# Kernel tuning notes

Measured on AMD Instinct MI355X. Metric: run time of the kernel, lower is better.

## Reference

```python
import jax, jax.numpy as jnp
import numpy as np

BIT, RW, CW, YR, ID, ZC = 4, 8, 8, 512, 64, 512


def setup_inputs() -> dict:
    key = jax.random.key(0)
    ks = jax.random.split(key, 8)
    return {
        "X": jax.random.normal(ks[0], (4096, CW * ZC), dtype=jnp.float32),
        "Y": jax.random.uniform(ks[1], (BIT, RW, CW, YR, ID), dtype=jnp.float32),
        "Z": jax.random.uniform(ks[2], (BIT, RW, CW, ID, ZC), dtype=jnp.float32),
        "a": jax.random.normal(ks[3], (BIT, RW, CW, 1, 1), dtype=jnp.float32),
        "b": jax.random.normal(ks[4], (BIT, RW, CW, 1, 1), dtype=jnp.float32),
        "c": jax.random.normal(ks[5], (BIT, RW, CW, 1, 1), dtype=jnp.float32),
        "d": jax.random.normal(ks[6], (RW, CW, 1, 1), dtype=jnp.float32),
        "bias": jax.random.normal(ks[7], (RW * YR,), dtype=jnp.float32),
    }


def reference(X, Y, Z, a, b, c, d, bias):
    dtype = X.dtype
    # binary codebook buffers (registered as bool in torch): threshold at 0.5
    Yb = (Y > 0.5).astype(dtype)  # [bit, rw, cw, y_row, inter]
    Zb = (Z > 0.5).astype(dtype)  # [bit, rw, cw, inter, z_col]
    # batched binary matmul: [bit, rw, cw, y_row, z_col]
    W_core = jnp.einsum('brcyi,brciz->brcyz', Yb, Zb)
    Y_sum = jnp.sum(Yb, axis=-1, keepdims=True)  # [bit, rw, cw, y_row, 1]
    Z_sum = jnp.sum(Zb, axis=-2, keepdims=True)  # [bit, rw, cw, 1, z_col]
    W = a * W_core + b * Y_sum + c * Z_sum       # [bit, rw, cw, y_row, z_col]
    W = jnp.sum(W, axis=0) + d                   # [rw, cw, y_row, z_col]
    # permute(0,2,1,3) -> [rw, y_row, cw, z_col] -> [rw*y_row, cw*z_col]
    W = jnp.transpose(W, (0, 2, 1, 3)).reshape(RW * YR, CW * ZC)
    return X @ W.T + bias
```

## Files before the change

kernel.cpp:

```cpp
#include <hip/hip_runtime.h>

#define KDIM 4096
#define MDIM 4096
#define GAS __attribute__((address_space(1)))
#define LAS __attribute__((address_space(3)))

typedef __attribute__((ext_vector_type(8))) _Float16 f16x8;
typedef __attribute__((ext_vector_type(4))) float f32x4;

__device__ __forceinline__ unsigned short f2h(float v) {
    return __builtin_bit_cast(unsigned short, (_Float16)v);
}

__global__ __launch_bounds__(256) void pack_y_kernel(
    const float* __restrict__ Y, unsigned long long* __restrict__ Ym) {
    const int g = blockIdx.x * 4 + (threadIdx.x >> 6);
    const int lane = threadIdx.x & 63;
    float v = Y[(size_t)g * 64 + lane];
    unsigned long long m = __ballot(v > 0.5f);
    if (lane == 0) Ym[g] = m;
}

__global__ __launch_bounds__(512) void pack_z_kernel(
    const float* __restrict__ Z, unsigned long long* __restrict__ Zm) {
    const int s = blockIdx.x;
    const int z = threadIdx.x;
    const size_t base = (size_t)s * 64 * 512;
    unsigned long long m = 0;
#pragma unroll
    for (int i = 0; i < 64; ++i) {
        float v = Z[base + (size_t)i * 512 + z];
        m |= (unsigned long long)(v > 0.5f) << i;
    }
    Zm[(size_t)s * 512 + z] = m;
}

__global__ __launch_bounds__(512) void build_w_kernel(
    const unsigned long long* __restrict__ Ym, const unsigned long long* __restrict__ Zm,
    const float* __restrict__ Ac, const float* __restrict__ Bc,
    const float* __restrict__ Cc, const float* __restrict__ Dc,
    unsigned short* __restrict__ Wh) {
    const int rc = blockIdx.x;
    const int rw = rc >> 3, cw = rc & 7;
    const int yc = blockIdx.y;
    const int tid = threadIdx.x;
    const int zq = tid & 127;
    const int ys = tid >> 7;

    __shared__ unsigned long long sYm[4][16];

    float Ar[4], Br[4];
    float dval = Dc[rc];
    float czd4[4] = {dval, dval, dval, dval};
    unsigned long long zm[4][4];
#pragma unroll
    for (int b = 0; b < 4; ++b) {
        Ar[b] = Ac[b * 64 + rc];
        Br[b] = Bc[b * 64 + rc];
        float cb = Cc[b * 64 + rc];
        const unsigned long long* zp = Zm + (size_t)(b * 64 + rc) * 512 + zq * 4;
#pragma unroll
        for (int j = 0; j < 4; ++j) {
            zm[b][j] = zp[j];
            czd4[j] += cb * (float)__popcll(zm[b][j]);
        }
    }
    if (tid < 64)
        sYm[tid >> 4][tid & 15] = Ym[(size_t)((tid >> 4) * 64 + rc) * 512 + yc * 16 + (tid & 15)];
    __syncthreads();

#pragma unroll
    for (int yy = 0; yy < 4; ++yy) {
        const int yl = ys * 4 + yy;
        unsigned long long ym[4];
        float bt = 0.f;
#pragma unroll
        for (int b = 0; b < 4; ++b) {
            ym[b] = sYm[b][yl];
            bt += Br[b] * (float)__popcll(ym[b]);
        }
        ushort4 o4;
        float w0 = bt + czd4[0], w1 = bt + czd4[1], w2 = bt + czd4[2], w3 = bt + czd4[3];
#pragma unroll
        for (int b = 0; b < 4; ++b) {
            w0 += Ar[b] * (float)__popcll(ym[b] & zm[b][0]);
            w1 += Ar[b] * (float)__popcll(ym[b] & zm[b][1]);
            w2 += Ar[b] * (float)__popcll(ym[b] & zm[b][2]);
            w3 += Ar[b] * (float)__popcll(ym[b] & zm[b][3]);
        }
        o4.x = f2h(w0); o4.y = f2h(w1); o4.z = f2h(w2); o4.w = f2h(w3);
        size_t o = (size_t)(rw * 512 + yc * 16 + yl) * KDIM + cw * 512 + zq * 4;
        *reinterpret_cast<ushort4*>(&Wh[o]) = o4;
    }
}

__global__ __launch_bounds__(256) void convert_x_kernel(
    const float* __restrict__ X, unsigned short* __restrict__ Xh) {
    const size_t i = (size_t)blockIdx.x * 256 + threadIdx.x;
    float4 v = reinterpret_cast<const float4*>(X)[i];
    ushort4 h;
    h.x = f2h(v.x); h.y = f2h(v.y); h.z = f2h(v.z); h.w = f2h(v.w);
    reinterpret_cast<ushort4*>(Xh)[i] = h;
}

__global__ __launch_bounds__(512) void gemm_f16_kernel(
    const unsigned short* __restrict__ Xh, const unsigned short* __restrict__ Wh,
    const float* __restrict__ bias, float* __restrict__ out) {
    extern __shared__ unsigned short smem[];

    const int tid = threadIdx.x;
    const int lane = tid & 63;
    const int wave = tid >> 6;
    const int wr = wave >> 2, wc = wave & 3;
    const int fr = lane & 15, fq = lane >> 4;

    const int bid = blockIdx.x;
    const int swz = (bid & 7) * 32 + (bid >> 3);
    const int bx = swz & 15, by = swz >> 4;
    const int row0 = by * 256, col0 = bx * 256;

    int goff[2];
#pragma unroll
    for (int uh = 0; uh < 2; ++uh) {
        int d = uh * 8192 + tid * 16;
        int e = d ^ (((d >> 7) & 7) << 4);
        int rowl = ((e >> 7) << 1) | ((e >> 6) & 1);
        int kel = (e >> 1) & 31;
        goff[uh] = rowl * KDIM + kel;
    }

    const int sw = (fr >> 1) << 3;
    int idxA[8], idxB[4];
#pragma unroll
    for (int m = 0; m < 8; ++m)
        idxA[m] = ((wr * 64 + m * 8 + (fr >> 1)) * 64 + (fr & 1) * 32 + fq * 8) ^ sw;
#pragma unroll
    for (int n = 0; n < 4; ++n)
        idxB[n] = ((wc * 32 + n * 8 + (fr >> 1)) * 64 + (fr & 1) * 32 + fq * 8) ^ sw;

    const unsigned short* Abase = Xh + (size_t)row0 * KDIM;
    const unsigned short* Bbase = Wh + (size_t)col0 * KDIM;
    const int ldsw = wave * 512;

    f32x4 acc[8][4] = {};

#pragma unroll
    for (int t = 0; t < 3; ++t) {
        const int ub = t * 16384;
#pragma unroll
        for (int uh = 0; uh < 2; ++uh) {
            __builtin_amdgcn_global_load_lds((GAS void*)(Abase + t * 32 + goff[uh]),
                (LAS void*)(smem + ub + uh * 4096 + ldsw), 16, 0, 0);
            __builtin_amdgcn_global_load_lds((GAS void*)(Bbase + t * 32 + goff[uh]),
                (LAS void*)(smem + ub + 8192 + uh * 4096 + ldsw), 16, 0, 0);
        }
    }
    asm volatile("s_waitcnt vmcnt(8)" ::: "memory");
    __builtin_amdgcn_s_barrier();

    int cb = 0;
    for (int t = 0; t < 128; ++t) {
        const int nb = (cb + 49152) & 65535;
        const int tk = (t < 125) ? (t + 3) * 32 : 0;

        f16x8 a0[4], bfr[4];
#pragma unroll
        for (int m = 0; m < 4; ++m) a0[m] = *reinterpret_cast<const f16x8*>(&smem[cb + idxA[m]]);
#pragma unroll
        for (int n = 0; n < 4; ++n) bfr[n] = *reinterpret_cast<const f16x8*>(&smem[cb + 8192 + idxB[n]]);
#pragma unroll
        for (int uh = 0; uh < 2; ++uh)
            __builtin_amdgcn_global_load_lds((GAS void*)(Abase + tk + goff[uh]),
                (LAS void*)(smem + nb + uh * 4096 + ldsw), 16, 0, 0);
        __builtin_amdgcn_s_barrier();
        __builtin_amdgcn_s_setprio(1);
#pragma unroll
        for (int m = 0; m < 4; ++m)
#pragma unroll
            for (int n = 0; n < 4; ++n)
                acc[m][n] = __builtin_amdgcn_mfma_f32_16x16x32_f16(a0[m], bfr[n], acc[m][n], 0, 0, 0);
        __builtin_amdgcn_s_setprio(0);
        __builtin_amdgcn_s_barrier();

        f16x8 a1[4];
#pragma unroll
        for (int m = 0; m < 4; ++m) a1[m] = *reinterpret_cast<const f16x8*>(&smem[cb + idxA[4 + m]]);
#pragma unroll
        for (int uh = 0; uh < 2; ++uh)
            __builtin_amdgcn_global_load_lds((GAS void*)(Bbase + tk + goff[uh]),
                (LAS void*)(smem + nb + 8192 + uh * 4096 + ldsw), 16, 0, 0);
        __builtin_amdgcn_s_barrier();
        __builtin_amdgcn_s_setprio(1);
#pragma unroll
        for (int m = 0; m < 4; ++m)
#pragma unroll
            for (int n = 0; n < 4; ++n)
                acc[4 + m][n] = __builtin_amdgcn_mfma_f32_16x16x32_f16(a1[m], bfr[n], acc[4 + m][n], 0, 0, 0);
        __builtin_amdgcn_s_setprio(0);
        asm volatile("s_waitcnt vmcnt(8)" ::: "memory");
        __builtin_amdgcn_s_barrier();

        cb = (cb + 16384) & 65535;
    }
    asm volatile("s_waitcnt vmcnt(0)" ::: "memory");

    float bv[4];
#pragma unroll
    for (int n = 0; n < 4; ++n) bv[n] = bias[col0 + wc * 64 + n * 16 + fr];

#pragma unroll
    for (int m = 0; m < 8; ++m) {
        const int orow = row0 + wr * 128 + m * 16 + fq * 4;
#pragma unroll
        for (int n = 0; n < 4; ++n) {
            const int ocol = col0 + wc * 64 + n * 16 + fr;
            float* po = out + (size_t)orow * MDIM + ocol;
#pragma unroll
            for (int e = 0; e < 4; ++e)
                po[(size_t)e * MDIM] = acc[m][n][e] + bv[n];
        }
    }
}

extern "C" void kernel_launch(void* const* d_in, const int* in_sizes, int n_in,
                              void* d_out, int out_size, void* d_ws, size_t ws_size,
                              hipStream_t stream) {
    const float* X  = (const float*)d_in[0];
    const float* Y  = (const float*)d_in[1];
    const float* Z  = (const float*)d_in[2];
    const float* Ac = (const float*)d_in[3];
    const float* Bc = (const float*)d_in[4];
    const float* Cc = (const float*)d_in[5];
    const float* Dc = (const float*)d_in[6];
    const float* bias = (const float*)d_in[7];
    float* out = (float*)d_out;

    char* ws = (char*)d_ws;
    unsigned short* Xh = (unsigned short*)(ws);
    unsigned short* Wh = (unsigned short*)(ws + (size_t)33554432);
    unsigned long long* Ym = (unsigned long long*)(ws + (size_t)67108864);
    unsigned long long* Zm = (unsigned long long*)(ws + (size_t)68157440);

    pack_y_kernel<<<32768, 256, 0, stream>>>(Y, Ym);
    pack_z_kernel<<<256, 512, 0, stream>>>(Z, Zm);
    build_w_kernel<<<dim3(64, 32), 512, 0, stream>>>(Ym, Zm, Ac, Bc, Cc, Dc, Wh);
    convert_x_kernel<<<16384, 256, 0, stream>>>(X, Xh);
    gemm_f16_kernel<<<dim3(256), 512, 131072, stream>>>(Xh, Wh, bias, out);
}
```

Before: 336.8 us.

## Merge pack kernels, grid-stride X conversion, drop mid-iteration GEMM barriers

```diff
diff --git a/kernel.cpp b/kernel.cpp
--- a/kernel.cpp
+++ b/kernel.cpp
@@ -12,27 +12,29 @@
     return __builtin_bit_cast(unsigned short, (_Float16)v);
 }
 
-__global__ __launch_bounds__(256) void pack_y_kernel(
-    const float* __restrict__ Y, unsigned long long* __restrict__ Ym) {
-    const int g = blockIdx.x * 4 + (threadIdx.x >> 6);
-    const int lane = threadIdx.x & 63;
-    float v = Y[(size_t)g * 64 + lane];
-    unsigned long long m = __ballot(v > 0.5f);
-    if (lane == 0) Ym[g] = m;
-}
-
-__global__ __launch_bounds__(512) void pack_z_kernel(
-    const float* __restrict__ Z, unsigned long long* __restrict__ Zm) {
-    const int s = blockIdx.x;
-    const int z = threadIdx.x;
-    const size_t base = (size_t)s * 64 * 512;
-    unsigned long long m = 0;
-#pragma unroll
-    for (int i = 0; i < 64; ++i) {
-        float v = Z[base + (size_t)i * 512 + z];
-        m |= (unsigned long long)(v > 0.5f) << i;
-    }
-    Zm[(size_t)s * 512 + z] = m;
+__global__ __launch_bounds__(256) void pack_yz_kernel(
+    const float* __restrict__ Y, const float* __restrict__ Z,
+    unsigned long long* __restrict__ Ym, unsigned long long* __restrict__ Zm) {
+    const int bid = blockIdx.x;
+    const int tid = threadIdx.x;
+    if (bid < 32768) {
+        const int g = bid * 4 + (tid >> 6);
+        const int lane = tid & 63;
+        float v = Y[(size_t)g * 64 + lane];
+        unsigned long long m = __ballot(v > 0.5f);
+        if (lane == 0) Ym[g] = m;
+    } else {
+        const int s = (bid - 32768) >> 1;
+        const int z = ((bid - 32768) & 1) * 256 + tid;
+        const size_t base = (size_t)s * 64 * 512;
+        unsigned long long m = 0;
+#pragma unroll
+        for (int i = 0; i < 64; ++i) {
+            float v = Z[base + (size_t)i * 512 + z];
+            m |= (unsigned long long)(v > 0.5f) << i;
+        }
+        Zm[(size_t)s * 512 + z] = m;
+    }
 }
 
 __global__ __launch_bounds__(512) void build_w_kernel(
@@ -96,11 +98,15 @@
 
 __global__ __launch_bounds__(256) void convert_x_kernel(
     const float* __restrict__ X, unsigned short* __restrict__ Xh) {
-    const size_t i = (size_t)blockIdx.x * 256 + threadIdx.x;
-    float4 v = reinterpret_cast<const float4*>(X)[i];
-    ushort4 h;
-    h.x = f2h(v.x); h.y = f2h(v.y); h.z = f2h(v.z); h.w = f2h(v.w);
-    reinterpret_cast<ushort4*>(Xh)[i] = h;
+    const int nthr = 2048 * 256;
+    int i = blockIdx.x * 256 + threadIdx.x;
+#pragma unroll
+    for (int r = 0; r < 8; ++r, i += nthr) {
+        float4 v = reinterpret_cast<const float4*>(X)[i];
+        ushort4 h;
+        h.x = f2h(v.x); h.y = f2h(v.y); h.z = f2h(v.z); h.w = f2h(v.w);
+        reinterpret_cast<ushort4*>(Xh)[i] = h;
+    }
 }
 
 __global__ __launch_bounds__(512) void gemm_f16_kernel(
@@ -163,7 +169,7 @@
         const int nb = (cb + 49152) & 65535;
         const int tk = (t < 125) ? (t + 3) * 32 : 0;
 
-        f16x8 a0[4], bfr[4];
+        f16x8 a0[4], a1[4], bfr[4];
 #pragma unroll
         for (int m = 0; m < 4; ++m) a0[m] = *reinterpret_cast<const f16x8*>(&smem[cb + idxA[m]]);
 #pragma unroll
@@ -172,31 +178,26 @@
         for (int uh = 0; uh < 2; ++uh)
             __builtin_amdgcn_global_load_lds((GAS void*)(Abase + tk + goff[uh]),
                 (LAS void*)(smem + nb + uh * 4096 + ldsw), 16, 0, 0);
-        __builtin_amdgcn_s_barrier();
-        __builtin_amdgcn_s_setprio(1);
-#pragma unroll
-        for (int m = 0; m < 4; ++m)
-#pragma unroll
-            for (int n = 0; n < 4; ++n)
-                acc[m][n] = __builtin_amdgcn_mfma_f32_16x16x32_f16(a0[m], bfr[n], acc[m][n], 0, 0, 0);
-        __builtin_amdgcn_s_setprio(0);
-        __builtin_amdgcn_s_barrier();
-
-        f16x8 a1[4];
 #pragma unroll
         for (int m = 0; m < 4; ++m) a1[m] = *reinterpret_cast<const f16x8*>(&smem[cb + idxA[4 + m]]);
 #pragma unroll
         for (int uh = 0; uh < 2; ++uh)
             __builtin_amdgcn_global_load_lds((GAS void*)(Bbase + tk + goff[uh]),
                 (LAS void*)(smem + nb + 8192 + uh * 4096 + ldsw), 16, 0, 0);
-        __builtin_amdgcn_s_barrier();
+
         __builtin_amdgcn_s_setprio(1);
+#pragma unroll
+        for (int m = 0; m < 4; ++m)
+#pragma unroll
+            for (int n = 0; n < 4; ++n)
+                acc[m][n] = __builtin_amdgcn_mfma_f32_16x16x32_f16(a0[m], bfr[n], acc[m][n], 0, 0, 0);
 #pragma unroll
         for (int m = 0; m < 4; ++m)
 #pragma unroll
             for (int n = 0; n < 4; ++n)
                 acc[4 + m][n] = __builtin_amdgcn_mfma_f32_16x16x32_f16(a1[m], bfr[n], acc[4 + m][n], 0, 0, 0);
         __builtin_amdgcn_s_setprio(0);
+
         asm volatile("s_waitcnt vmcnt(8)" ::: "memory");
         __builtin_amdgcn_s_barrier();
 
@@ -241,9 +242,8 @@
     unsigned long long* Ym = (unsigned long long*)(ws + (size_t)67108864);
     unsigned long long* Zm = (unsigned long long*)(ws + (size_t)68157440);
 
-    pack_y_kernel<<<32768, 256, 0, stream>>>(Y, Ym);
-    pack_z_kernel<<<256, 512, 0, stream>>>(Z, Zm);
+    pack_yz_kernel<<<33280, 256, 0, stream>>>(Y, Z, Ym, Zm);
     build_w_kernel<<<dim3(64, 32), 512, 0, stream>>>(Ym, Zm, Ac, Bc, Cc, Dc, Wh);
-    convert_x_kernel<<<16384, 256, 0, stream>>>(X, Xh);
+    convert_x_kernel<<<2048, 256, 0, stream>>>(X, Xh);
     gemm_f16_kernel<<<dim3(256), 512, 131072, stream>>>(Xh, Wh, bias, out);
 }
```

Measured after the change: 340.7 us. Within noise of the previous version (+1.1%).
